# Kernel optimization log

Hardware: AMD Instinct MI355X
Metric: run time of the kernel (lower is better)

The kernel has to match this reference:

```python
import jax, jax.numpy as jnp
import numpy as np

TWO_PI = 2.0 * np.pi
B, S_IN, S_OUT, K, HID = 1024, 4096, 4096, 8, 512
EPS = 1e-6


def setup_inputs() -> dict:
    key = jax.random.key(0)
    k1, k2, k3, k4, k5, k6, k7, k8 = jax.random.split(key, 8)
    x_in = jax.random.uniform(k1, (B, S_OUT), dtype=jnp.float32) * TWO_PI
    x_passive = jax.random.normal(k2, (B, S_IN), dtype=jnp.float32)
    log_density = jax.random.normal(k3, (B, 1), dtype=jnp.float32)
    # MLP params (nn.Linear default-ish init scale)
    lim1 = 1.0 / np.sqrt(S_IN)
    lim2 = 1.0 / np.sqrt(HID)
    w1 = jax.random.uniform(k4, (S_IN, HID), jnp.float32, -lim1, lim1)
    b1 = jax.random.uniform(k5, (HID,), jnp.float32, -lim1, lim1)
    w2 = jax.random.uniform(k6, (HID, S_OUT * 3 * K), jnp.float32, -lim2, lim2)
    b2 = jax.random.uniform(k7, (S_OUT * 3 * K,), jnp.float32, -lim2, lim2)
    phase_shift = jax.random.uniform(k8, (1,), jnp.float32)
    return {"x_in": x_in, "x_passive": x_passive, "log_density": log_density,
            "w1": w1, "b1": b1, "w2": w2, "b2": b2, "phase_shift": phase_shift}


def reference(x_in, x_passive, log_density, w1, b1, w2, b2, phase_shift):
    # normalise network input with global mean / (unbiased) std, as torch does
    xn = (x_passive - x_passive.mean()) / x_passive.std(ddof=1)
    # dense network: Linear -> tanh -> Linear -> tanh (final_activation=activation)
    net = jnp.tanh(jnp.tanh(xn @ w1 + b1) @ w2 + b2)            # (B, S*3K)
    net = net.reshape(-1, S_OUT, 3 * K)
    h_raw, w_raw, d_raw = net[..., :K], net[..., K:2 * K], net[..., 2 * K:]
    h_norm = jax.nn.softmax(h_raw, axis=2) * TWO_PI              # (B,S,K)
    w_norm = jax.nn.softmax(w_raw, axis=2) * TWO_PI
    d_norm = jax.nn.softplus(d_raw)
    bshape = (h_norm.shape[0], S_OUT, 1)
    x_kp = jnp.concatenate([jnp.full(bshape, -EPS, h_norm.dtype),
                            jnp.cumsum(w_norm, axis=2)], axis=2)  # (B,S,K+1)
    phi_kp = jnp.concatenate([jnp.zeros(bshape, h_norm.dtype),
                              jnp.cumsum(h_norm, axis=2)], axis=2)
    x = x_in[..., None]                                          # (B,S,1)
    # searchsorted (left) per element: count of knots strictly less than x, minus 1
    k_ind = jnp.sum(x_kp < x, axis=2, keepdims=True) - 1         # (B,S,1) int
    k_ind = jnp.clip(k_ind, 0, K - 1)
    g = lambda a, i: jnp.take_along_axis(a, i, axis=2)
    w_k = g(w_norm, k_ind)
    h_k = g(h_norm, k_ind)
    s_k = h_k / w_k
    d_k = g(d_norm, k_ind)
    d_kp1 = g(d_norm, (k_ind + 1) % K)
    x_km1 = g(x_kp, k_ind)
    phi_km1 = g(phi_kp, k_ind)
    alpha = (x - x_km1) / w_k
    a1m = alpha * (1.0 - alpha)
    denom = s_k + (d_kp1 + d_k - 2.0 * s_k) * a1m
    phi_out = (phi_km1 + h_k * (s_k * alpha ** 2 + d_k * a1m) / denom)[..., 0]
    phi_out = (phi_out + phase_shift) % TWO_PI                   # (B,S)
    grad = s_k ** 2 * (d_kp1 * alpha ** 2 + 2.0 * s_k * a1m
                       + d_k * (1.0 - alpha) ** 2) / denom ** 2  # (B,S,1)
    log_density = log_density - jnp.log(grad).sum(axis=1)        # (B,1)
    return phi_out, log_density
```

## Files before the change

### kernel.cpp

```cpp
#include <hip/hip_runtime.h>
#include <cstdint>
#include <cstddef>


typedef unsigned short u16;
typedef __bf16 bf16x8 __attribute__((ext_vector_type(8)));
typedef float f32x4 __attribute__((ext_vector_type(4)));
typedef unsigned short u16x8 __attribute__((ext_vector_type(8)));
typedef unsigned short u16x4 __attribute__((ext_vector_type(4)));
typedef unsigned short u16x2 __attribute__((ext_vector_type(2)));

#define TWOPI_F 6.28318530717958647692f

static __device__ __forceinline__ u16 f32_to_bf16(float f){
  unsigned u = __builtin_bit_cast(unsigned, f);
  return (u16)((u + 0x7fffu + ((u >> 16) & 1u)) >> 16);
}
static __device__ __forceinline__ void async16(void* lds, const void* g){
  __builtin_amdgcn_global_load_lds((const __attribute__((address_space(1))) void*)g,
                                   (__attribute__((address_space(3))) void*)lds,
                                   16, 0, 0);
}
static __device__ __forceinline__ float fast_tanh(float x){
  x = fminf(fmaxf(x, -15.f), 15.f);
  float e = __expf(2.f * x);
  return (e - 1.f) / (e + 1.f);
}
static __device__ __forceinline__ float softplus_f(float x){
  return fmaxf(x, 0.f) + __logf(1.f + __expf(-fabsf(x)));
}

__global__ void k_stats(const float* __restrict__ xp, float* __restrict__ stats){
  __shared__ float ss[4], sq[4];
  const int tid = threadIdx.x;
  const long gt = (long)blockIdx.x * 256 + tid;
  const float4* x4 = (const float4*)xp;
  float s = 0.f, q = 0.f;
  #pragma unroll
  for (int p = 0; p < 4; ++p){
    float4 v = x4[gt + (long)p * 262144];
    s += v.x + v.y + v.z + v.w;
    q += v.x*v.x + v.y*v.y + v.z*v.z + v.w*v.w;
  }
  #pragma unroll
  for (int off = 32; off; off >>= 1){
    s += __shfl_down(s, off);
    q += __shfl_down(q, off);
  }
  if ((tid & 63) == 0){ ss[tid>>6] = s; sq[tid>>6] = q; }
  __syncthreads();
  if (tid == 0){
    atomicAdd(stats,     ss[0]+ss[1]+ss[2]+ss[3]);
    atomicAdd(stats + 1, sq[0]+sq[1]+sq[2]+sq[3]);
  }
}

__global__ void k_prep(const float* __restrict__ xp, const float* __restrict__ stats,
                       u16* __restrict__ xn){
  const long t = (long)blockIdx.x * 256 + threadIdx.x;
  const float sum = stats[0], sq = stats[1];
  const float N = 4194304.f;
  const float mean = sum / N;
  const float istd = rsqrtf((sq - sum*sum/N) / (N - 1.f));
  const float4* x4 = (const float4*)xp;
  const float4 a = x4[2*t], b = x4[2*t+1];
  u16x8 o;
  o[0]=f32_to_bf16((a.x-mean)*istd); o[1]=f32_to_bf16((a.y-mean)*istd);
  o[2]=f32_to_bf16((a.z-mean)*istd); o[3]=f32_to_bf16((a.w-mean)*istd);
  o[4]=f32_to_bf16((b.x-mean)*istd); o[5]=f32_to_bf16((b.y-mean)*istd);
  o[6]=f32_to_bf16((b.z-mean)*istd); o[7]=f32_to_bf16((b.w-mean)*istd);
  ((u16x8*)xn)[t] = o;
}

__global__ __launch_bounds__(256) void k_transpose_cvt(const float* __restrict__ in,
                                                       u16* __restrict__ out,
                                                       int Kd, int Nd){
  __shared__ __align__(16) u16 tT[128*256];
  const int tid = threadIdx.x;
  const long k0 = (long)blockIdx.x * 256, n0 = (long)blockIdx.y * 128;
  const int lam = tid & 31, g = tid >> 5;
  const int c = lam * 4;
  const int sig = (lam & 7) << 2;
  #pragma unroll
  for (int pass = 0; pass < 16; ++pass){
    const int P = pass*8 + g;
    const float4 f0 = *(const float4*)&in[(k0 + 2*P    )*Nd + n0 + c];
    const float4 f1 = *(const float4*)&in[(k0 + 2*P + 1)*Nd + n0 + c];
    const int pp = 2*(P ^ sig);
    *(u16x2*)&tT[(c    )*256 + pp] = u16x2{f32_to_bf16(f0.x), f32_to_bf16(f1.x)};
    *(u16x2*)&tT[(c + 1)*256 + pp] = u16x2{f32_to_bf16(f0.y), f32_to_bf16(f1.y)};
    *(u16x2*)&tT[(c + 2)*256 + pp] = u16x2{f32_to_bf16(f0.z), f32_to_bf16(f1.z)};
    *(u16x2*)&tT[(c + 3)*256 + pp] = u16x2{f32_to_bf16(f0.w), f32_to_bf16(f1.w)};
  }
  __syncthreads();
  const int w = tid >> 6, l = tid & 63;
  const int lh = l >> 5, lk = l & 31;
  #pragma unroll
  for (int it = 0; it < 16; ++it){
    const int n = (w << 5) + (it << 1) + lh;
    const int s2 = (n >> 2) & 7;
    const u16x8 v = *(const u16x8*)&tT[n*256 + 8*(lk ^ s2)];
    *(u16x8*)&out[(n0 + n)*Kd + k0 + 8*lk] = v;
  }
}

__global__ __launch_bounds__(256, 2) void k_gemm1(
    const u16* __restrict__ xn,
    const u16* __restrict__ w1t,
    float* __restrict__ pp)
{
  __shared__ __align__(16) u16 sA[64*32];
  __shared__ __align__(16) u16 sB[64*32];
  const int tid = threadIdx.x, lane = tid & 63, w = tid >> 6;
  const int n0 = blockIdx.x << 6, m0 = blockIdx.y << 6;
  const int ks = blockIdx.z;
  const int wm = w >> 1, wn = w & 1;
  const int rA = lane >> 2, cA = (lane & 3) << 3;
  const int fr = lane & 15, fq = lane >> 4;
  const f32x4 z4 = {0.f, 0.f, 0.f, 0.f};
  f32x4 acc[2][2];
  #pragma unroll
  for (int i=0;i<2;i++){ acc[i][0] = z4; acc[i][1] = z4; }

  for (int kt = 0; kt < 64; ++kt){
    const int kofs = (ks << 11) + (kt << 5) + cA;
    async16(sA + w*512, xn  + (long)(m0 + w*16 + rA)*4096 + kofs);
    async16(sB + w*512, w1t + (long)(n0 + w*16 + rA)*4096 + kofs);
    __syncthreads();
    bf16x8 af[2], bfv[2];
    #pragma unroll
    for (int i=0;i<2;i++) af[i]  = *(const bf16x8*)(sA + ((wm<<5) + i*16 + fr)*32 + (fq<<3));
    #pragma unroll
    for (int j=0;j<2;j++) bfv[j] = *(const bf16x8*)(sB + ((wn<<5) + j*16 + fr)*32 + (fq<<3));
    #pragma unroll
    for (int i=0;i<2;i++)
      #pragma unroll
      for (int j=0;j<2;j++)
        acc[i][j] = __builtin_amdgcn_mfma_f32_16x16x32_bf16(af[i], bfv[j], acc[i][j], 0, 0, 0);
    __syncthreads();
  }
  float* po = pp + ((size_t)ks << 19);
  #pragma unroll
  for (int i=0;i<2;i++)
    #pragma unroll
    for (int j=0;j<2;j++)
      #pragma unroll
      for (int r=0;r<4;r++){
        const int row = m0 + (wm<<5) + i*16 + (fq<<2) + r;
        const int col = n0 + (wn<<5) + j*16 + fr;
        po[row*512 + col] = acc[i][j][r];
      }
}

__global__ void k_gemm1b(const float* __restrict__ pp, const float* __restrict__ b1,
                         u16* __restrict__ hb){
  const int t = blockIdx.x * 256 + threadIdx.x;
  const float4 a = ((const float4*)pp)[t];
  const float4 b = ((const float4*)pp)[131072 + t];
  const float4 bb = ((const float4*)b1)[t & 127];
  u16x4 o;
  o[0] = f32_to_bf16(fast_tanh(a.x + b.x + bb.x));
  o[1] = f32_to_bf16(fast_tanh(a.y + b.y + bb.y));
  o[2] = f32_to_bf16(fast_tanh(a.z + b.z + bb.z));
  o[3] = f32_to_bf16(fast_tanh(a.w + b.w + bb.w));
  ((u16x4*)hb)[t] = o;
}

__global__ __launch_bounds__(256, 2) void k_gemm2(
    const u16* __restrict__ hmat,
    const u16* __restrict__ w2t,
    const float* __restrict__ b2,
    const float* __restrict__ x_in,
    const float* __restrict__ phase,
    float* __restrict__ phi_out,
    float* __restrict__ part)
{
  __shared__ __align__(16) char smem[25600];
  u16* sA = (u16*)smem;
  u16* sB = (u16*)(smem + 16384);
  float* sC = (float*)smem;

  const int tid  = threadIdx.x;
  const int lane = tid & 63;
  const int w    = tid >> 6;
  const int nt   = blockIdx.y;
  const int m0   = blockIdx.x << 8;
  const long n0  = (long)nt * 96;

  const int rA = lane >> 2, cA = (lane & 3) << 3;
  const int fr = lane & 15, fq = lane >> 4;

  const f32x4 z4 = {0.f, 0.f, 0.f, 0.f};
  f32x4 acc[4][6];
  #pragma unroll
  for (int i=0;i<4;i++)
    #pragma unroll
    for (int j=0;j<6;j++) acc[i][j] = z4;

  for (int kt = 0; kt < 16; ++kt){
    const int kofs = (kt << 5) + cA;
    #pragma unroll
    for (int cc = 0; cc < 4; ++cc){
      const int c = (w << 2) + cc;
      async16(sA + c*512, hmat + (long)(m0 + c*16 + rA)*512 + kofs);
    }
    #pragma unroll
    for (int cc = 0; cc < 2; ++cc){
      const int ch = (w << 1) + cc;
      int row = ch*16 + rA; if (row > 95) row = 95;
      async16(sB + ch*512, w2t + (n0 + row)*512 + kofs);
    }
    __syncthreads();
    bf16x8 af[4], bfv[6];
    #pragma unroll
    for (int i=0;i<4;i++)
      af[i] = *(const bf16x8*)(sA + ((w<<6) + i*16 + fr)*32 + (fq<<3));
    #pragma unroll
    for (int j=0;j<6;j++)
      bfv[j] = *(const bf16x8*)(sB + (j*16 + fr)*32 + (fq<<3));
    #pragma unroll
    for (int i=0;i<4;i++)
      #pragma unroll
      for (int j=0;j<6;j++)
        acc[i][j] = __builtin_amdgcn_mfma_f32_16x16x32_bf16(af[i], bfv[j], acc[i][j], 0, 0, 0);
    __syncthreads();
  }

  const float shift = phase[0];
  float b2c[6];
  #pragma unroll
  for (int j=0;j<6;j++) b2c[j] = b2[n0 + j*16 + fr];
  float* myC = sC + w*1600;

  #pragma unroll
  for (int q = 0; q < 4; ++q){
    __syncthreads();
    #pragma unroll
    for (int j=0;j<6;j++)
      #pragma unroll
      for (int r=0;r<4;r++)
        myC[((fq<<2)+r)*100 + j*16 + fr] = fast_tanh(acc[q][j][r] + b2c[j]);
    __syncthreads();

    const int row = fr;
    const int g   = fq;
    const float* tp = myC + row*100 + g*24;
    float t[24];
    #pragma unroll
    for (int jj=0;jj<24;jj++) t[jj] = tp[jj];

    const int bg = m0 + (w<<6) + (q<<4) + row;
    const int s  = (nt<<2) + g;
    const float x = x_in[(long)bg*4096 + s];

    float eh[8], ew[8];
    float sh = 0.f, sw = 0.f;
    #pragma unroll
    for (int i=0;i<8;i++){ eh[i] = __expf(t[i]);   sh += eh[i]; }
    #pragma unroll
    for (int i=0;i<8;i++){ ew[i] = __expf(t[8+i]); sw += ew[i]; }
    const float fh = TWOPI_F / sh, fw = TWOPI_F / sw;

    float cw = 0.f; int k = 0;
    #pragma unroll
    for (int i=0;i<8;i++){ cw += ew[i]*fw; k += (cw < x) ? 1 : 0; }
    if (k > 7) k = 7;

    float xkm1 = -1e-6f, ph = 0.f, wk = 0.f, hk = 0.f, dr0 = 0.f, dr1 = 0.f;
    float cw2 = 0.f, chs = 0.f;
    #pragma unroll
    for (int i=0;i<8;i++){
      const float wi = ew[i]*fw, hi = eh[i]*fh;
      if (i == k){
        wk = wi; hk = hi;
        xkm1 = (i == 0) ? -1e-6f : cw2;
        ph = chs;
        dr0 = t[16 + i];
        dr1 = t[16 + ((i+1)&7)];
      }
      cw2 += wi; chs += hi;
    }
    const float dk  = softplus_f(dr0);
    const float dk1 = softplus_f(dr1);
    const float sk  = hk / wk;
    const float alpha = (x - xkm1) / wk;
    const float a1m = alpha * (1.f - alpha);
    const float denom = sk + (dk1 + dk - 2.f*sk)*a1m;
    const float phiv = ph + hk*(sk*alpha*alpha + dk*a1m)/denom;
    float p = phiv + shift;
    if (p >= TWOPI_F) p -= TWOPI_F;
    if (p >= TWOPI_F) p -= TWOPI_F;
    phi_out[(long)bg*4096 + s] = p;

    const float om = 1.f - alpha;
    const float num = dk1*alpha*alpha + 2.f*sk*a1m + dk*om*om;
    float lg = __logf(sk*sk*num/(denom*denom));
    lg += __shfl_xor(lg, 16);
    lg += __shfl_xor(lg, 32);
    if (lane < 16) part[(long)bg*1024 + nt] = lg;
  }
}

__global__ void k_ldred(const float* __restrict__ part, const float* __restrict__ ldin,
                        float* __restrict__ ldout){
  __shared__ float ss[4];
  const int b = blockIdx.x, tid = threadIdx.x;
  const float4* p4 = (const float4*)(part + ((long)b << 10));
  const float4 v = p4[tid];
  float s = v.x + v.y + v.z + v.w;
  #pragma unroll
  for (int off = 32; off; off >>= 1) s += __shfl_down(s, off);
  if ((tid & 63) == 0) ss[tid >> 6] = s;
  __syncthreads();
  if (tid == 0) ldout[b] = ldin[b] - (ss[0]+ss[1]+ss[2]+ss[3]);
}

extern "C" void kernel_launch(void* const* d_in, const int* in_sizes, int n_in,
                              void* d_out, int out_size, void* d_ws, size_t ws_size,
                              hipStream_t stream){
  (void)in_sizes; (void)n_in; (void)out_size; (void)ws_size;
  const float* x_in  = (const float*)d_in[0];
  const float* x_pas = (const float*)d_in[1];
  const float* ldin  = (const float*)d_in[2];
  const float* w1    = (const float*)d_in[3];
  const float* b1    = (const float*)d_in[4];
  const float* w2    = (const float*)d_in[5];
  const float* b2    = (const float*)d_in[6];
  const float* phase = (const float*)d_in[7];
  float* out   = (float*)d_out;
  float* phi   = out;
  float* ldout = out + (size_t)1024*4096;

  char* ws = (char*)d_ws;
  float* stats = (float*)ws;
  u16* xn   = (u16*)(ws + 256);
  u16* w1t  = (u16*)(ws + 8388864);
  u16* hb   = (u16*)(ws + 12583168);
  u16* w2t  = (u16*)(ws + 13631744);
  float* part = (float*)(ws + 114295040);

  hipMemsetAsync(stats, 0, 8, stream);
  k_stats<<<1024, 256, 0, stream>>>(x_pas, stats);
  k_prep<<<2048, 256, 0, stream>>>(x_pas, stats, xn);
  k_transpose_cvt<<<dim3(16, 4),  256, 0, stream>>>(w1, w1t, 4096, 512);
  k_transpose_cvt<<<dim3(2, 768), 256, 0, stream>>>(w2, w2t, 512, 98304);
  k_gemm1<<<dim3(8, 16, 2), 256, 0, stream>>>(xn, w1t, part);
  k_gemm1b<<<512, 256, 0, stream>>>(part, b1, hb);
  k_gemm2<<<dim3(4, 1024), 256, 0, stream>>>(hb, w2t, b2, x_in, phase, phi, part);
  k_ldred<<<1024, 256, 0, stream>>>(part, ldin, ldout);
}
```

Measured before the change: 571.8 us.

## Multi-buffer LDS staging in both GEMMs and drop epilogue block barriers

GEMM1 gets a four-slot LDS ring with loads issued two K-steps ahead. GEMM2 gets two LDS buffers, loading the next K-tile while the current one feeds the MFMAs. Both use explicit vmcnt waits and one s_barrier per step instead of two __syncthreads, so global-to-LDS latency overlaps with compute. The GEMM2 epilogue also drops its per-quarter block barriers, since each wave only touches its own scratch region, and reads that scratch as 16-byte vectors. The cost is more shared memory per block (GEMM2 goes to 48 KB), which could cut occupancy, and the hand-written waitcnt counts must match the number of loads in flight.

```diff
diff --git a/kernel.cpp b/kernel.cpp
--- a/kernel.cpp
+++ b/kernel.cpp
@@ -109,8 +109,8 @@
     const u16* __restrict__ w1t,
     float* __restrict__ pp)
 {
-  __shared__ __align__(16) u16 sA[64*32];
-  __shared__ __align__(16) u16 sB[64*32];
+  __shared__ __align__(16) u16 sA[4][64*32];
+  __shared__ __align__(16) u16 sB[4][64*32];
   const int tid = threadIdx.x, lane = tid & 63, w = tid >> 6;
   const int n0 = blockIdx.x << 6, m0 = blockIdx.y << 6;
   const int ks = blockIdx.z;
@@ -122,22 +122,35 @@
   #pragma unroll
   for (int i=0;i<2;i++){ acc[i][0] = z4; acc[i][1] = z4; }
 
+  auto stage = [&](int kt){
+    const int b = kt & 3;
+    const int kofs = (ks << 11) + (kt << 5) + cA;
+    async16(sA[b] + w*512, xn  + (long)(m0 + w*16 + rA)*4096 + kofs);
+    async16(sB[b] + w*512, w1t + (long)(n0 + w*16 + rA)*4096 + kofs);
+  };
+
+  stage(0); stage(1);
   for (int kt = 0; kt < 64; ++kt){
-    const int kofs = (ks << 11) + (kt << 5) + cA;
-    async16(sA + w*512, xn  + (long)(m0 + w*16 + rA)*4096 + kofs);
-    async16(sB + w*512, w1t + (long)(n0 + w*16 + rA)*4096 + kofs);
-    __syncthreads();
+    if (kt < 62){
+      stage(kt + 2);
+      asm volatile("s_waitcnt vmcnt(4)" ::: "memory");
+    } else if (kt == 62){
+      asm volatile("s_waitcnt vmcnt(2)" ::: "memory");
+    } else {
+      asm volatile("s_waitcnt vmcnt(0)" ::: "memory");
+    }
+    __builtin_amdgcn_s_barrier();
+    const int b = kt & 3;
     bf16x8 af[2], bfv[2];
     #pragma unroll
-    for (int i=0;i<2;i++) af[i]  = *(const bf16x8*)(sA + ((wm<<5) + i*16 + fr)*32 + (fq<<3));
-    #pragma unroll
-    for (int j=0;j<2;j++) bfv[j] = *(const bf16x8*)(sB + ((wn<<5) + j*16 + fr)*32 + (fq<<3));
+    for (int i=0;i<2;i++) af[i]  = *(const bf16x8*)(sA[b] + ((wm<<5) + i*16 + fr)*32 + (fq<<3));
+    #pragma unroll
+    for (int j=0;j<2;j++) bfv[j] = *(const bf16x8*)(sB[b] + ((wn<<5) + j*16 + fr)*32 + (fq<<3));
     #pragma unroll
     for (int i=0;i<2;i++)
       #pragma unroll
       for (int j=0;j<2;j++)
         acc[i][j] = __builtin_amdgcn_mfma_f32_16x16x32_bf16(af[i], bfv[j], acc[i][j], 0, 0, 0);
-    __syncthreads();
   }
   float* po = pp + ((size_t)ks << 19);
   #pragma unroll
@@ -175,10 +188,7 @@
     float* __restrict__ phi_out,
     float* __restrict__ part)
 {
-  __shared__ __align__(16) char smem[25600];
-  u16* sA = (u16*)smem;
-  u16* sB = (u16*)(smem + 16384);
-  float* sC = (float*)smem;
+  __shared__ __align__(16) char smem[49152];
 
   const int tid  = threadIdx.x;
   const int lane = tid & 63;
@@ -197,35 +207,52 @@
     #pragma unroll
     for (int j=0;j<6;j++) acc[i][j] = z4;
 
-  for (int kt = 0; kt < 16; ++kt){
+  auto stage = [&](int kt, int b){
     const int kofs = (kt << 5) + cA;
+    u16* bA = (u16*)(smem + b*24576);
+    u16* bB = (u16*)(smem + b*24576 + 16384);
     #pragma unroll
     for (int cc = 0; cc < 4; ++cc){
       const int c = (w << 2) + cc;
-      async16(sA + c*512, hmat + (long)(m0 + c*16 + rA)*512 + kofs);
+      async16(bA + c*512, hmat + (long)(m0 + c*16 + rA)*512 + kofs);
     }
     #pragma unroll
     for (int cc = 0; cc < 2; ++cc){
       const int ch = (w << 1) + cc;
       int row = ch*16 + rA; if (row > 95) row = 95;
-      async16(sB + ch*512, w2t + (n0 + row)*512 + kofs);
-    }
-    __syncthreads();
+      async16(bB + ch*512, w2t + (n0 + row)*512 + kofs);
+    }
+  };
+
+  stage(0, 0);
+  #pragma unroll 2
+  for (int kt = 0; kt < 16; ++kt){
+    const int cur = kt & 1;
+    if (kt < 15){
+      stage(kt + 1, cur ^ 1);
+      asm volatile("s_waitcnt vmcnt(6)" ::: "memory");
+    } else {
+      asm volatile("s_waitcnt vmcnt(0)" ::: "memory");
+    }
+    __builtin_amdgcn_s_barrier();
+    const u16* bA = (const u16*)(smem + cur*24576);
+    const u16* bB = (const u16*)(smem + cur*24576 + 16384);
     bf16x8 af[4], bfv[6];
     #pragma unroll
     for (int i=0;i<4;i++)
-      af[i] = *(const bf16x8*)(sA + ((w<<6) + i*16 + fr)*32 + (fq<<3));
+      af[i] = *(const bf16x8*)(bA + ((w<<6) + i*16 + fr)*32 + (fq<<3));
     #pragma unroll
     for (int j=0;j<6;j++)
-      bfv[j] = *(const bf16x8*)(sB + (j*16 + fr)*32 + (fq<<3));
+      bfv[j] = *(const bf16x8*)(bB + (j*16 + fr)*32 + (fq<<3));
     #pragma unroll
     for (int i=0;i<4;i++)
       #pragma unroll
       for (int j=0;j<6;j++)
         acc[i][j] = __builtin_amdgcn_mfma_f32_16x16x32_bf16(af[i], bfv[j], acc[i][j], 0, 0, 0);
-    __syncthreads();
-  }
-
+    __builtin_amdgcn_s_barrier();
+  }
+
+  float* sC = (float*)smem;
   const float shift = phase[0];
   float b2c[6];
   #pragma unroll
@@ -234,20 +261,21 @@
 
   #pragma unroll
   for (int q = 0; q < 4; ++q){
-    __syncthreads();
     #pragma unroll
     for (int j=0;j<6;j++)
       #pragma unroll
       for (int r=0;r<4;r++)
         myC[((fq<<2)+r)*100 + j*16 + fr] = fast_tanh(acc[q][j][r] + b2c[j]);
-    __syncthreads();
 
     const int row = fr;
     const int g   = fq;
-    const float* tp = myC + row*100 + g*24;
+    const f32x4* tp4 = (const f32x4*)(myC + row*100 + g*24);
     float t[24];
     #pragma unroll
-    for (int jj=0;jj<24;jj++) t[jj] = tp[jj];
+    for (int jj=0;jj<6;jj++){
+      const f32x4 v = tp4[jj];
+      t[4*jj] = v[0]; t[4*jj+1] = v[1]; t[4*jj+2] = v[2]; t[4*jj+3] = v[3];
+    }
 
     const int bg = m0 + (w<<6) + (q<<4) + row;
     const int s  = (nt<<2) + g;
```

Measured after the change: 571.5 us. No clear change (-0.1%).
